# Optimization experiments

Measured on AMD Instinct MI355X. Metric: run time of the kernel, lower is better.

The kernel has to match this reference:

```python
import jax, jax.numpy as jnp
import numpy as np

E = 1024   # embed_dim
H = 8      # att_heads
HD = E // H
L = 4      # layer_num
B = 64
M = 256
EPS = 1e-5


def celu(x, alpha=1.3):
    return jnp.where(x > 0, x, alpha * jnp.expm1(x / alpha))


def group_norm(x, w, b):
    # x: [N, E], groups = H (GroupNorm over channel groups, per-sample)
    xg = x.reshape(-1, H, HD)
    mu = xg.mean(-1, keepdims=True)
    var = ((xg - mu) ** 2).mean(-1, keepdims=True)
    xg = (xg - mu) * jax.lax.rsqrt(var + EPS)
    return xg.reshape(-1, E) * w + b


def layer_norm(x, w, b):
    mu = x.mean(-1, keepdims=True)
    var = ((x - mu) ** 2).mean(-1, keepdims=True)
    return (x - mu) * jax.lax.rsqrt(var + EPS) * w + b


def setup_inputs() -> dict:
    key = jax.random.key(0)
    ks = jax.random.split(key, 20)
    s = 0.02
    return {
        "gv_feat": jnp.zeros((B, 1), jnp.float32),
        "att_feats": jax.random.normal(ks[0], (B, M, E), jnp.float32),
        "att_mask": jnp.ones((B, M), jnp.float32),
        "mem_W": jax.random.normal(ks[1], (L, E, E), jnp.float32) * s,
        "mem_b": jnp.zeros((L, E), jnp.float32),
        "gn_w": jnp.ones((L, E), jnp.float32),
        "gn_b": jnp.zeros((L, E), jnp.float32),
        "upd_W": jax.random.normal(ks[2], (L, 2 * HD, HD), jnp.float32) * s,
        "upd_b": jnp.zeros((L, HD), jnp.float32),
        "gate_W": jax.random.normal(ks[3], (L, 2 * HD, HD), jnp.float32) * s,
        "gate_b": jnp.zeros((L, HD), jnp.float32),
        "ln_w": jnp.ones((L, E), jnp.float32),
        "ln_b": jnp.zeros((L, E), jnp.float32),
        "proj_W": jax.random.normal(ks[4], ((L + 1) * E, E), jnp.float32) * s,
        "proj_b": jnp.zeros((E,), jnp.float32),
        "lnf_w": jnp.ones((E,), jnp.float32),
        "lnf_b": jnp.zeros((E,), jnp.float32),
    }


def reference(gv_feat, att_feats, att_mask, mem_W, mem_b, gn_w, gn_b,
              upd_W, upd_b, gate_W, gate_b, ln_w, ln_b,
              proj_W, proj_b, lnf_w, lnf_b):
    scaling = HD ** (-0.5)
    mask3 = att_mask[:, :, None]                       # [B, M, 1]
    msum = mask3.sum(1)                                # [B, 1]

    def pool(x):
        return (x * mask3).sum(1) / msum               # [B, E]

    # gv_feat has last dim 1 -> computed by masked mean pooling
    gv = pool(att_feats)
    feat_arr = [gv]
    x = att_feats
    key_mask = att_mask[:, None, None, :]              # [B, 1, 1, M]
    for i in range(L):
        mem = celu(x.reshape(-1, E) @ mem_W[i] + mem_b[i])
        mem = group_norm(mem, gn_w[i], gn_b[i])
        xh = x.reshape(B, M, H, HD).swapaxes(1, 2)     # [B, H, M, HD]
        mh = mem.reshape(B, M, H, HD).swapaxes(1, 2)   # [B, H, M, HD]
        attn = jnp.einsum('bhqd,bhkd->bhqk', xh, mh) * scaling
        attn = jnp.where(key_mask == 0, -1e9, attn)
        p = jax.nn.softmax(attn, axis=-1)
        ctx = jnp.einsum('bhqk,bhkd->bhqd', p, xh)     # values == xh
        inp = jnp.concatenate([xh, ctx], axis=-1)      # [B, H, M, 2*HD]
        f_t = jnp.tanh(jax.nn.relu(inp @ upd_W[i] + upd_b[i]))  # dropout = eval identity
        g_t = jax.nn.sigmoid(inp @ gate_W[i] + gate_b[i])
        xh = g_t * f_t + (1.0 - g_t) * xh
        x = xh.swapaxes(1, 2).reshape(B, M, E)
        x = layer_norm(x, ln_w[i], ln_b[i])
        feat_arr.append(pool(x))
    gv = jnp.concatenate(feat_arr, axis=-1) @ proj_W + proj_b
    gv = layer_norm(gv, lnf_w, lnf_b)
    return gv, x
```

## Files before the change

### kernel.cpp

```cpp
#include <hip/hip_runtime.h>
#include <hip/hip_bf16.h>
#include <cstdint>
#include <cstddef>

typedef __bf16 v8bf __attribute__((ext_vector_type(8)));
typedef __bf16 v4bf __attribute__((ext_vector_type(4)));
typedef float  f32x4 __attribute__((ext_vector_type(4)));

typedef __attribute__((address_space(1))) void gas_void;
typedef __attribute__((address_space(3))) void las_void;

__device__ __forceinline__ void gload_lds16(const void* g, void* l) {
  __builtin_amdgcn_global_load_lds((const gas_void*)g, (las_void*)l, 16, 0, 0);
}

__device__ __forceinline__ float rdv(const void* p, size_t idx, int isf) {
  return isf ? ((const float*)p)[idx] : (float)((const __bf16*)p)[idx];
}

#define PB 64
#define PM 256
#define PE 1024
#define PH 8
#define PHD 128

__global__ void detect_kernel(const void* mask, int* flags) {
  if (threadIdx.x == 0) {
    uint32_t w = *(const uint32_t*)mask;
    flags[0] = ((w >> 16) == 0x3F80u && (w & 0xFFFFu) == 0x3F80u) ? 0 : 1;
  }
}

__global__ __launch_bounds__(256) void convx_kernel(
    const void* __restrict__ src, const int* __restrict__ flags, __bf16* __restrict__ dst) {
  const size_t i = ((size_t)blockIdx.x * 256 + threadIdx.x) * 4;
  if (flags[0]) {
    const float* s = (const float*)src + i;
    v4bf o; o[0] = (__bf16)s[0]; o[1] = (__bf16)s[1]; o[2] = (__bf16)s[2]; o[3] = (__bf16)s[3];
    *(v4bf*)(dst + i) = o;
  } else {
    *(v4bf*)(dst + i) = *(const v4bf*)((const __bf16*)src + i);
  }
}

__global__ __launch_bounds__(256) void transpose_kernel(
    const void* __restrict__ src, size_t soff, size_t zsrc, const int* __restrict__ flags,
    __bf16* __restrict__ dst, size_t zdst, int K, int N) {
  __shared__ __bf16 tile[64][66];
  const int isf = flags[0];
  const size_t so = soff + (size_t)blockIdx.z * zsrc;
  __bf16* d = dst + (size_t)blockIdx.z * zdst;
  const int n0 = blockIdx.x * 64, k0 = blockIdx.y * 64;
  const int c = threadIdx.x & 63, r0 = threadIdx.x >> 6;
#pragma unroll
  for (int j = 0; j < 16; ++j) {
    const int r = j * 4 + r0;
    tile[r][c] = (__bf16)rdv(src, so + (size_t)(k0 + r) * N + (n0 + c), isf);
  }
  __syncthreads();
#pragma unroll
  for (int j = 0; j < 16; ++j) {
    const int r = j * 4 + r0;
    d[(size_t)(n0 + r) * K + k0 + c] = tile[c][r];
  }
}

__global__ __launch_bounds__(256) void ugtr_kernel(
    const void* __restrict__ updW, const void* __restrict__ gateW,
    const int* __restrict__ flags, __bf16* __restrict__ ugWt) {
  __shared__ __bf16 tile[64][66];
  const int isf = flags[0];
  const int z = blockIdx.z, i = z >> 1, g = z & 1;
  const void* src = g ? gateW : updW;
  const size_t soff = (size_t)i * 32768;
  __bf16* dst = ugWt + (size_t)i * 65536 + g * 32768;
  const int n0 = blockIdx.x * 64, k0 = blockIdx.y * 64;
  const int c = threadIdx.x & 63, r0 = threadIdx.x >> 6;
#pragma unroll
  for (int j = 0; j < 16; ++j) {
    const int r = j * 4 + r0;
    tile[r][c] = (__bf16)rdv(src, soff + (size_t)(k0 + r) * 128 + (n0 + c), isf);
  }
  __syncthreads();
#pragma unroll
  for (int j = 0; j < 16; ++j) {
    const int r = j * 4 + r0;
    dst[(size_t)(n0 + r) * 256 + k0 + c] = tile[c][r];
  }
}

template<int AMODE, int BMODE, int ACT, bool OUTF32, bool CLAMPM, bool GNF, bool SPLITK, bool SWZ>
__global__ __launch_bounds__(512) void gemm_kernel(
    const __bf16* __restrict__ A, const __bf16* __restrict__ A2,
    const __bf16* __restrict__ Bt,
    const void* __restrict__ bias_a, int offa, const void* __restrict__ bias_b, int offb,
    int bias_split, const int* __restrict__ flags,
    const void* __restrict__ gnw, const void* __restrict__ gnb, int gnoff,
    void* __restrict__ Cout, int K, int Kfull, int Ntot, int Mtot)
{
  __shared__ __align__(16) uint8_t a_s[2][32768];
  __shared__ __align__(16) uint8_t b_s[2][16384];
  __shared__ float gnsum[256][2];
  __shared__ float gnsq[256][2];
  int bx = blockIdx.x, by = blockIdx.y;
  if (SWZ) {
    const int nx = gridDim.x;
    const int flat = by * nx + bx;
    const int xcd = flat & 7, slot = flat >> 3;
    by = slot & 7;
    bx = (slot >> 3) * 8 + xcd;
  }
  const int mbase = bx * 256;
  const int nbase = by * 128;
  const int koff = SPLITK ? blockIdx.z * K : 0;
  const int tid = threadIdx.x;
  const int wid = tid >> 6, lane = tid & 63;
  const int wr = wid >> 1, wc = wid & 1;

  f32x4 acc[4][4];
#pragma unroll
  for (int m = 0; m < 4; ++m)
#pragma unroll
    for (int n = 0; n < 4; ++n) acc[m][n] = (f32x4){0.f, 0.f, 0.f, 0.f};

  const int nkt = K >> 6;
  const int lrow8 = lane >> 3;
  const int cc = (lane & 7) << 4;

  auto STAGE = [&](int kt, uint8_t* as, uint8_t* bs) {
    const int kbase = koff + (kt << 6);
#pragma unroll
    for (int j = 0; j < 4; ++j) {
      const int q = wid * 4 + j;
      const int row = q * 8 + lrow8;
      const int c = cc ^ ((row & 7) << 4);
      const int klocal = c >> 1;
      const __bf16* asrc;
      if (AMODE == 0) {
        int rg = mbase + row;
        if (CLAMPM && rg > Mtot - 1) rg = Mtot - 1;
        asrc = A + (size_t)rg * Kfull + (kbase + klocal);
      } else {
        const int rg = mbase + row;
        const int kg = kbase + klocal;
        if (kg < PHD) {
          const int bh = rg >> 8, mm = rg & 255;
          const int bb = bh >> 3, hh = bh & 7;
          asrc = A + ((size_t)(bb * PM + mm) * PE + hh * PHD + kg);
        } else {
          asrc = A2 + ((size_t)rg * PHD + (kg - PHD));
        }
      }
      gload_lds16(asrc, as + q * 1024);
    }
#pragma unroll
    for (int j = 0; j < 2; ++j) {
      const int q = wid * 2 + j;
      const int row = q * 8 + lrow8;
      const int c = cc ^ ((row & 7) << 4);
      const int klocal = c >> 1;
      const __bf16* bsrc;
      if (BMODE == 0) {
        bsrc = Bt + (size_t)(nbase + row) * Kfull + (kbase + klocal);
      } else {
        bsrc = Bt + (size_t)(mbase >> 8) * (PHD * PM)
                  + (size_t)(nbase + row) * Kfull + (kbase + klocal);
      }
      gload_lds16(bsrc, bs + q * 1024);
    }
  };

  STAGE(0, a_s[0], b_s[0]);
  if (nkt > 1) STAGE(1, a_s[1], b_s[1]);

  for (int kt = 0; kt < nkt; ++kt) {
    if (kt + 1 < nkt) asm volatile("s_waitcnt vmcnt(6)" ::: "memory");
    else              asm volatile("s_waitcnt vmcnt(0)" ::: "memory");
    __builtin_amdgcn_s_barrier();
    __builtin_amdgcn_sched_barrier(0);
    const uint8_t* ap = a_s[kt & 1];
    const uint8_t* bp = b_s[kt & 1];
#pragma unroll
    for (int kk = 0; kk < 2; ++kk) {
      const int co = kk * 64 + ((lane >> 4) << 4);
      v8bf af[4], bfr[4];
#pragma unroll
      for (int m = 0; m < 4; ++m) {
        const int row = wr * 64 + m * 16 + (lane & 15);
        af[m] = *(const v8bf*)(ap + row * 128 + (co ^ ((row & 7) << 4)));
      }
#pragma unroll
      for (int n = 0; n < 4; ++n) {
        const int row = wc * 64 + n * 16 + (lane & 15);
        bfr[n] = *(const v8bf*)(bp + row * 128 + (co ^ ((row & 7) << 4)));
      }
#pragma unroll
      for (int m = 0; m < 4; ++m)
#pragma unroll
        for (int n = 0; n < 4; ++n)
          acc[m][n] = __builtin_amdgcn_mfma_f32_16x16x32_bf16(af[m], bfr[n], acc[m][n], 0, 0, 0);
    }
    __builtin_amdgcn_s_barrier();
    __builtin_amdgcn_sched_barrier(0);
    if (kt + 2 < nkt) STAGE(kt + 2, a_s[kt & 1], b_s[kt & 1]);
  }

  const int isf = flags[0];
  if constexpr (GNF) {
    float bv[4];
#pragma unroll
    for (int n = 0; n < 4; ++n) {
      const int col = nbase + wc * 64 + n * 16 + (lane & 15);
      bv[n] = (bias_a != nullptr) ? rdv(bias_a, offa + col, isf) : 0.f;
    }
#pragma unroll
    for (int m = 0; m < 4; ++m)
#pragma unroll
      for (int n = 0; n < 4; ++n)
#pragma unroll
        for (int r = 0; r < 4; ++r) {
          float v = acc[m][n][r] + bv[n];
          if (ACT == 1) v = (v > 0.f) ? v : 1.3f * expm1f(v * (1.0f / 1.3f));
          acc[m][n][r] = v;
        }
#pragma unroll
    for (int m = 0; m < 4; ++m)
#pragma unroll
      for (int r = 0; r < 4; ++r) {
        float s = 0.f, q = 0.f;
#pragma unroll
        for (int n = 0; n < 4; ++n) { s += acc[m][n][r]; q += acc[m][n][r] * acc[m][n][r]; }
#pragma unroll
        for (int off = 1; off < 16; off <<= 1) {
          s += __shfl_xor(s, off, 64); q += __shfl_xor(q, off, 64);
        }
        const int lrow = wr * 64 + m * 16 + ((lane >> 4) << 2) + r;
        if ((lane & 15) == 0) { gnsum[lrow][wc] = s; gnsq[lrow][wc] = q; }
      }
    __syncthreads();
#pragma unroll
    for (int m = 0; m < 4; ++m)
#pragma unroll
      for (int r = 0; r < 4; ++r) {
        const int lrow = wr * 64 + m * 16 + ((lane >> 4) << 2) + r;
        const float mean = (gnsum[lrow][0] + gnsum[lrow][1]) * (1.f / 128.f);
        const float var = (gnsq[lrow][0] + gnsq[lrow][1]) * (1.f / 128.f) - mean * mean;
        const float rstd = rsqrtf(var + 1e-5f);
        const int rg = mbase + lrow;
#pragma unroll
        for (int n = 0; n < 4; ++n) {
          const int col = nbase + wc * 64 + n * 16 + (lane & 15);
          const float o = (acc[m][n][r] - mean) * rstd * rdv(gnw, gnoff + col, isf)
                          + rdv(gnb, gnoff + col, isf);
          ((__bf16*)Cout)[(size_t)rg * Ntot + col] = (__bf16)o;
        }
      }
  } else {
    float* coutF = (float*)Cout + (SPLITK ? (size_t)blockIdx.z * 65536 : (size_t)0);
#pragma unroll
    for (int m = 0; m < 4; ++m) {
      const int rowt = mbase + wr * 64 + m * 16 + ((lane >> 4) << 2);
#pragma unroll
      for (int n = 0; n < 4; ++n) {
        const int col = nbase + wc * 64 + n * 16 + (lane & 15);
        float bvv = 0.f;
        if (bias_a != nullptr)
          bvv = (col < bias_split) ? rdv(bias_a, offa + col, isf)
                                   : rdv(bias_b, offb + col - bias_split, isf);
#pragma unroll
        for (int r = 0; r < 4; ++r) {
          const int rg = rowt + r;
          if (CLAMPM && rg >= Mtot) continue;
          float v = acc[m][n][r] + bvv;
          if (ACT == 1) v = (v > 0.f) ? v : 1.3f * expm1f(v * (1.0f / 1.3f));
          if (OUTF32) coutF[(size_t)rg * Ntot + col] = v;
          else        ((__bf16*)Cout)[(size_t)rg * Ntot + col] = (__bf16)v;
        }
      }
    }
  }
}

__global__ __launch_bounds__(256) void attn_softmax_kernel(
    const __bf16* __restrict__ xc, const __bf16* __restrict__ memc,
    const void* __restrict__ mask, const int* __restrict__ flags, int b0,
    __bf16* __restrict__ S)
{
  const int bhl = blockIdx.x;
  const int bl = bhl >> 3, h = bhl & 7;
  const int isf = flags[0];
  const int tid = threadIdx.x, wid = tid >> 6, lane = tid & 63;
  const int qbase = blockIdx.y * 64 + wid * 16;
  const size_t xoff = (size_t)bl * PM * PE + h * PHD;

  v8bf a[4];
  {
    const int row = qbase + (lane & 15);
    const int d0 = (lane >> 4) * 8;
    const __bf16* p = xc + xoff + (size_t)row * PE + d0;
#pragma unroll
    for (int k = 0; k < 4; ++k) a[k] = *(const v8bf*)(p + k * 32);
  }
  float mz[16];
#pragma unroll
  for (int t = 0; t < 16; ++t)
    mz[t] = rdv(mask, (size_t)(b0 + bl) * PM + t * 16 + (lane & 15), isf);

  f32x4 acc[16];
#pragma unroll
  for (int t = 0; t < 16; ++t) acc[t] = (f32x4){0.f, 0.f, 0.f, 0.f};
#pragma unroll
  for (int t = 0; t < 16; ++t) {
    const int key = t * 16 + (lane & 15);
    const int d0 = (lane >> 4) * 8;
    const __bf16* p = memc + xoff + (size_t)key * PE + d0;
#pragma unroll
    for (int k = 0; k < 4; ++k) {
      v8bf bb = *(const v8bf*)(p + k * 32);
      acc[t] = __builtin_amdgcn_mfma_f32_16x16x32_bf16(a[k], bb, acc[t], 0, 0, 0);
    }
  }
  const float scale = 0.08838834764831845f;
  float mx[4], sm[4];
#pragma unroll
  for (int r = 0; r < 4; ++r) mx[r] = -3.0e38f;
#pragma unroll
  for (int t = 0; t < 16; ++t)
#pragma unroll
    for (int r = 0; r < 4; ++r) {
      float v = (mz[t] == 0.f) ? -1.0e9f : acc[t][r] * scale;
      acc[t][r] = v;
      mx[r] = fmaxf(mx[r], v);
    }
#pragma unroll
  for (int off = 1; off < 16; off <<= 1)
#pragma unroll
    for (int r = 0; r < 4; ++r) mx[r] = fmaxf(mx[r], __shfl_xor(mx[r], off, 64));
#pragma unroll
  for (int r = 0; r < 4; ++r) sm[r] = 0.f;
#pragma unroll
  for (int t = 0; t < 16; ++t)
#pragma unroll
    for (int r = 0; r < 4; ++r) {
      float e = expf(acc[t][r] - mx[r]);
      acc[t][r] = e; sm[r] += e;
    }
#pragma unroll
  for (int off = 1; off < 16; off <<= 1)
#pragma unroll
    for (int r = 0; r < 4; ++r) sm[r] += __shfl_xor(sm[r], off, 64);
#pragma unroll
  for (int r = 0; r < 4; ++r) sm[r] = 1.f / sm[r];

  const size_t srow = (size_t)bhl * PM;
#pragma unroll
  for (int r = 0; r < 4; ++r) {
    const int q = qbase + (lane >> 4) * 4 + r;
    __bf16* sp = S + (srow + q) * PM;
#pragma unroll
    for (int t = 0; t < 16; ++t)
      sp[t * 16 + (lane & 15)] = (__bf16)(acc[t][r] * sm[r]);
  }
}

__global__ __launch_bounds__(256) void transpose_x_kernel(
    const __bf16* __restrict__ xc, __bf16* __restrict__ xT)
{
  const int bh = blockIdx.x;
  const int b = bh >> 3, h = bh & 7;
  const int tz = blockIdx.y;
  const int d0 = (tz & 1) * 64, m0 = (tz >> 1) * 64;
  __shared__ __bf16 tile[64][66];
  const int c = threadIdx.x & 63, r0 = threadIdx.x >> 6;
  const __bf16* src = xc + ((size_t)b * PM + m0) * PE + h * PHD + d0;
#pragma unroll
  for (int j = 0; j < 16; ++j) {
    const int r = j * 4 + r0;
    tile[r][c] = src[(size_t)r * PE + c];
  }
  __syncthreads();
  __bf16* dst = xT + ((size_t)bh * PHD + d0) * PM + m0;
#pragma unroll
  for (int j = 0; j < 16; ++j) {
    const int r = j * 4 + r0;
    dst[(size_t)r * PM + c] = tile[c][r];
  }
}

__global__ __launch_bounds__(256) void gatingln_kernel(
    const __bf16* __restrict__ ug, const __bf16* __restrict__ xc,
    const void* __restrict__ w, const void* __restrict__ bz, int off,
    const int* __restrict__ flags, __bf16* __restrict__ xout,
    void* __restrict__ outAux, int row0)
{
  const size_t row = blockIdx.x;
  const int tid = threadIdx.x, wid = tid >> 6, lane = tid & 63;
  const int isf = flags[0];
  const int e = tid * 4, h = tid >> 5, d = e & 127;
  const size_t b = row >> 8; const int m = (int)(row & 255);
  const size_t ugrow = ((b * PH + h) * PM + m);
  v4bf fv = *(const v4bf*)(ug + ugrow * 256 + d);
  v4bf gvv = *(const v4bf*)(ug + ugrow * 256 + 128 + d);
  v4bf xv = *(const v4bf*)(xc + row * PE + e);
  float o[4];
#pragma unroll
  for (int r = 0; r < 4; ++r) {
    float f = fv[r], g = gvv[r], xh = xv[r];
    float gs = 1.f / (1.f + expf(-g));
    float ft = tanhf(fmaxf(f, 0.f));
    o[r] = gs * ft + (1.f - gs) * xh;
  }
  float s = o[0] + o[1] + o[2] + o[3];
  float q = o[0] * o[0] + o[1] * o[1] + o[2] * o[2] + o[3] * o[3];
#pragma unroll
  for (int off2 = 1; off2 < 64; off2 <<= 1) {
    s += __shfl_xor(s, off2, 64); q += __shfl_xor(q, off2, 64);
  }
  __shared__ float ss[4], qq[4];
  if (lane == 0) { ss[wid] = s; qq[wid] = q; }
  __syncthreads();
  s = ss[0] + ss[1] + ss[2] + ss[3];
  q = qq[0] + qq[1] + qq[2] + qq[3];
  const float mean = s * (1.f / 1024.f);
  const float var = q * (1.f / 1024.f) - mean * mean;
  const float rstd = rsqrtf(var + 1e-5f);
  float ov[4];
#pragma unroll
  for (int r = 0; r < 4; ++r)
    ov[r] = (o[r] - mean) * rstd * rdv(w, off + e + r, isf) + rdv(bz, off + e + r, isf);
  v4bf vo; vo[0] = (__bf16)ov[0]; vo[1] = (__bf16)ov[1]; vo[2] = (__bf16)ov[2]; vo[3] = (__bf16)ov[3];
  *(v4bf*)(xout + row * PE + e) = vo;
  if (outAux != nullptr) {
    const size_t idx = 65536 + (size_t)(row0 + row) * PE + e;
    if (isf) {
      float* op = (float*)outAux;
      op[idx] = ov[0]; op[idx + 1] = ov[1]; op[idx + 2] = ov[2]; op[idx + 3] = ov[3];
    } else {
      __bf16* op = (__bf16*)outAux;
      op[idx] = (__bf16)ov[0]; op[idx + 1] = (__bf16)ov[1];
      op[idx + 2] = (__bf16)ov[2]; op[idx + 3] = (__bf16)ov[3];
    }
  }
}

__global__ void msum_kernel(const void* __restrict__ mask, const int* __restrict__ flags,
                            float* __restrict__ msum)
{
  const int b = blockIdx.x, t = threadIdx.x;
  const int isf = flags[0];
  float s = 0.f;
#pragma unroll
  for (int j = 0; j < 4; ++j) s += rdv(mask, (size_t)b * PM + j * 64 + t, isf);
#pragma unroll
  for (int off = 1; off < 64; off <<= 1) s += __shfl_xor(s, off, 64);
  if (t == 0) msum[b] = s;
}

__global__ __launch_bounds__(1024) void pool_kernel(
    const __bf16* __restrict__ x, const void* __restrict__ mask, const int* __restrict__ flags,
    const float* __restrict__ msum, __bf16* __restrict__ feats, int colOff)
{
  __shared__ float red[4][256];
  const int b = blockIdx.x;
  const int el = threadIdx.x & 255;
  const int wq = threadIdx.x >> 8;
  const int e = blockIdx.y * 256 + el;
  const int isf = flags[0];
  const __bf16* p = x + (size_t)b * PM * PE + e;
  float acc = 0.f;
  const int m0 = wq * 64;
  for (int m = m0; m < m0 + 64; m += 4) {
#pragma unroll
    for (int j = 0; j < 4; ++j)
      acc += (float)p[(size_t)(m + j) * PE] * rdv(mask, (size_t)b * PM + m + j, isf);
  }
  red[wq][el] = acc;
  __syncthreads();
  if (wq == 0) {
    float s = red[0][el] + red[1][el] + red[2][el] + red[3][el];
    feats[(size_t)b * (5 * PE) + colOff + e] = (__bf16)(s / msum[b]);
  }
}

__global__ __launch_bounds__(256) void projreduce_kernel(
    const float* __restrict__ part, const void* __restrict__ pb,
    const int* __restrict__ flags, float* __restrict__ gvpre)
{
  const int row = blockIdx.x;
  const int c0 = threadIdx.x * 4;
  const int isf = flags[0];
  float a0 = rdv(pb, c0 + 0, isf), a1 = rdv(pb, c0 + 1, isf);
  float a2 = rdv(pb, c0 + 2, isf), a3 = rdv(pb, c0 + 3, isf);
#pragma unroll
  for (int z = 0; z < 8; ++z) {
    const float* p = part + (size_t)z * 65536 + (size_t)row * 1024 + c0;
    a0 += p[0]; a1 += p[1]; a2 += p[2]; a3 += p[3];
  }
  float* op = gvpre + (size_t)row * 1024 + c0;
  op[0] = a0; op[1] = a1; op[2] = a2; op[3] = a3;
}

__global__ __launch_bounds__(256) void ln_final_kernel(
    const float* __restrict__ gin, const void* __restrict__ w, const void* __restrict__ bz,
    const int* __restrict__ flags, void* __restrict__ out)
{
  const size_t row = blockIdx.x;
  const int tid = threadIdx.x, wid = tid >> 6, lane = tid & 63;
  const int isf = flags[0];
  const float* p = gin + row * PE + tid * 4;
  float f0 = p[0], f1 = p[1], f2 = p[2], f3 = p[3];
  float s = f0 + f1 + f2 + f3;
  float q = f0 * f0 + f1 * f1 + f2 * f2 + f3 * f3;
#pragma unroll
  for (int off = 1; off < 64; off <<= 1) {
    s += __shfl_xor(s, off, 64); q += __shfl_xor(q, off, 64);
  }
  __shared__ float ss[4], qq[4];
  if (lane == 0) { ss[wid] = s; qq[wid] = q; }
  __syncthreads();
  s = ss[0] + ss[1] + ss[2] + ss[3];
  q = qq[0] + qq[1] + qq[2] + qq[3];
  const float mean = s * (1.f / 1024.f);
  const float var = q * (1.f / 1024.f) - mean * mean;
  const float rstd = rsqrtf(var + 1e-5f);
  const int e = tid * 4;
#pragma unroll
  for (int j = 0; j < 4; ++j) {
    const float fj = (j == 0 ? f0 : j == 1 ? f1 : j == 2 ? f2 : f3);
    const float ov = (fj - mean) * rstd * rdv(w, e + j, isf) + rdv(bz, e + j, isf);
    if (isf) ((float*)out)[row * PE + e + j] = ov;
    else     ((__bf16*)out)[row * PE + e + j] = (__bf16)ov;
  }
}

extern "C" void kernel_launch(void* const* d_in, const int* in_sizes, int n_in,
                              void* d_out, int out_size, void* d_ws, size_t ws_size,
                              hipStream_t stream) {
  const void* att_feats = d_in[1];
  const void* att_mask  = d_in[2];
  const void* mem_W  = d_in[3];
  const void* mem_b  = d_in[4];
  const void* gn_w   = d_in[5];
  const void* gn_b   = d_in[6];
  const void* upd_W  = d_in[7];
  const void* upd_b  = d_in[8];
  const void* gate_W = d_in[9];
  const void* gate_b = d_in[10];
  const void* ln_w   = d_in[11];
  const void* ln_b   = d_in[12];
  const void* proj_W = d_in[13];
  const void* proj_b = d_in[14];
  const void* lnf_w  = d_in[15];
  const void* lnf_b  = d_in[16];

  uint8_t* ws = (uint8_t*)d_ws;
  int*    flags  = (int*)ws;
  float*  msum   = (float*)(ws + 4096);
  __bf16* featsb = (__bf16*)(ws + 8192);
  float*  gvpre  = (float*)(ws + 665600);
  __bf16* memWt  = (__bf16*)(ws + 1048576);
  __bf16* ugWt   = (__bf16*)(ws + 9437184);
  __bf16* xa0    = (__bf16*)(ws + 10485760);
  __bf16* xa     = (__bf16*)(ws + 44040192);
  uint8_t* dynb  = ws + 77594624;

  int NC;
  if (ws_size >= (size_t)211812352) NC = 1;
  else if (ws_size >= (size_t)144703488) NC = 2;
  else NC = 4;
  const int CSd = PB / NC;
  const int CROWSd = CSd * PM;
  const int CGRd = CSd * PH * PM;
  const size_t CB = (size_t)CROWSd * PE * 2;
  __bf16* membc = (__bf16*)dynb;
  __bf16* xTgc  = (__bf16*)(dynb + CB);
  __bf16* sbufc = (__bf16*)(dynb + 2 * CB);

  detect_kernel<<<1, 64, 0, stream>>>(att_mask, flags);
  convx_kernel<<<16384, 256, 0, stream>>>(att_feats, flags, xa0);

  transpose_kernel<<<dim3(16, 16, 4), 256, 0, stream>>>(
      mem_W, 0, 1048576, flags, memWt, 1048576, 1024, 1024);
  ugtr_kernel<<<dim3(2, 4, 8), 256, 0, stream>>>(upd_W, gate_W, flags, ugWt);

  msum_kernel<<<64, 64, 0, stream>>>(att_mask, flags, msum);
  pool_kernel<<<dim3(64, 4), 1024, 0, stream>>>(xa0, att_mask, flags, msum, featsb, 0);

  const __bf16* xcur = xa0;
  for (int i = 0; i < 4; ++i) {
    for (int c = 0; c < NC; ++c) {
      const __bf16* xc = xcur + (size_t)c * CROWSd * PE;
      gemm_kernel<0, 0, 1, false, false, true, false, true><<<dim3(CROWSd / 256, 8), 512, 0, stream>>>(
          xc, nullptr, memWt + (size_t)i * 1048576, mem_b, i * 1024, nullptr, 0, 1024,
          flags, gn_w, gn_b, i * 1024, membc, 1024, 1024, 1024, CROWSd);
      transpose_x_kernel<<<dim3(CSd * 8, 8), 256, 0, stream>>>(xc, xTgc);
      attn_softmax_kernel<<<dim3(CSd * 8, 4), 256, 0, stream>>>(xc, membc, att_mask, flags,
                                                                c * CSd, sbufc);
      gemm_kernel<0, 1, 0, false, false, false, false, false><<<dim3(CGRd / 256, 1), 512, 0, stream>>>(
          sbufc, nullptr, xTgc, nullptr, 0, nullptr, 0, 128, flags, nullptr, nullptr, 0,
          membc, 256, 256, 128, CGRd);
      gemm_kernel<1, 0, 0, false, false, false, false, false><<<dim3(CGRd / 256, 2), 512, 0, stream>>>(
          xc, membc, ugWt + (size_t)i * 65536, upd_b, i * 128, gate_b, i * 128, 128,
          flags, nullptr, nullptr, 0, sbufc, 256, 256, 256, CGRd);
      gatingln_kernel<<<CROWSd, 256, 0, stream>>>(sbufc, xc, ln_w, ln_b, i * 1024, flags,
                                                  xa + (size_t)c * CROWSd * PE,
                                                  (i == 3) ? d_out : nullptr, c * CROWSd);
    }
    pool_kernel<<<dim3(64, 4), 1024, 0, stream>>>(xa, att_mask, flags, msum, featsb,
                                                  (i + 1) * 1024);
    xcur = xa;
  }

  __bf16* projWt = sbufc;
  float* projPart = (float*)dynb;
  transpose_kernel<<<dim3(16, 80, 1), 256, 0, stream>>>(proj_W, 0, 0, flags, projWt, 0, 5120, 1024);
  gemm_kernel<0, 0, 0, true, true, false, true, false><<<dim3(1, 8, 8), 512, 0, stream>>>(
      featsb, nullptr, projWt, nullptr, 0, nullptr, 0, 1024,
      flags, nullptr, nullptr, 0, projPart, 640, 5120, 1024, 64);
  projreduce_kernel<<<64, 256, 0, stream>>>(projPart, proj_b, flags, gvpre);
  ln_final_kernel<<<64, 256, 0, stream>>>(gvpre, lnf_w, lnf_b, flags, d_out);
}
```

Before: 1.330 ms.

## Triple-buffer GEMM LDS and interleave staging with MFMA phases

Moves the bf16 GEMM from a double-buffered LDS pipeline to a triple-buffered one. Global-to-LDS staging for tile kt+2 is split into three parts and spread across four MFMA sub-phases, with s_setprio raising priority around the MFMA bursts. The wave layout changes from 4x2 waves with 64x64 tiles to 2x4 waves with 128x32 tiles. GroupNorm reduction scratch now aliases the B buffer, which keeps total LDS within limits. The aim is to hide global-load latency behind matrix math, at the cost of more barriers per k-step and slightly more LDS fragment reads per wave.

After: 1.635 ms. 1.23x slower.

```diff
diff --git a/kernel.cpp b/kernel.cpp
--- a/kernel.cpp
+++ b/kernel.cpp
@@ -98,10 +98,11 @@
     const void* __restrict__ gnw, const void* __restrict__ gnb, int gnoff,
     void* __restrict__ Cout, int K, int Kfull, int Ntot, int Mtot)
 {
-  __shared__ __align__(16) uint8_t a_s[2][32768];
-  __shared__ __align__(16) uint8_t b_s[2][16384];
-  __shared__ float gnsum[256][2];
-  __shared__ float gnsq[256][2];
+  __shared__ __align__(16) uint8_t a_s[3][32768];
+  __shared__ __align__(16) uint8_t b_s[3][16384];
+  float* gnS = (float*)&b_s[0][0];
+  float* gnQ = (float*)&b_s[0][4096];
+
   int bx = blockIdx.x, by = blockIdx.y;
   if (SWZ) {
     const int nx = gridDim.x;
@@ -115,108 +116,129 @@
   const int koff = SPLITK ? blockIdx.z * K : 0;
   const int tid = threadIdx.x;
   const int wid = tid >> 6, lane = tid & 63;
-  const int wr = wid >> 1, wc = wid & 1;
-
-  f32x4 acc[4][4];
-#pragma unroll
-  for (int m = 0; m < 4; ++m)
-#pragma unroll
-    for (int n = 0; n < 4; ++n) acc[m][n] = (f32x4){0.f, 0.f, 0.f, 0.f};
+  const int wr = wid >> 2, wc = wid & 3;
+
+  f32x4 acc[8][2];
+#pragma unroll
+  for (int m = 0; m < 8; ++m)
+#pragma unroll
+    for (int n = 0; n < 2; ++n) acc[m][n] = (f32x4){0.f, 0.f, 0.f, 0.f};
 
   const int nkt = K >> 6;
   const int lrow8 = lane >> 3;
   const int cc = (lane & 7) << 4;
 
-  auto STAGE = [&](int kt, uint8_t* as, uint8_t* bs) {
+  auto STAGE_PART = [&](int kt, int part, uint8_t* as, uint8_t* bs) {
     const int kbase = koff + (kt << 6);
-#pragma unroll
-    for (int j = 0; j < 4; ++j) {
-      const int q = wid * 4 + j;
-      const int row = q * 8 + lrow8;
-      const int c = cc ^ ((row & 7) << 4);
-      const int klocal = c >> 1;
-      const __bf16* asrc;
-      if (AMODE == 0) {
-        int rg = mbase + row;
-        if (CLAMPM && rg > Mtot - 1) rg = Mtot - 1;
-        asrc = A + (size_t)rg * Kfull + (kbase + klocal);
-      } else {
-        const int rg = mbase + row;
-        const int kg = kbase + klocal;
-        if (kg < PHD) {
-          const int bh = rg >> 8, mm = rg & 255;
-          const int bb = bh >> 3, hh = bh & 7;
-          asrc = A + ((size_t)(bb * PM + mm) * PE + hh * PHD + kg);
+    if (part < 2) {
+#pragma unroll
+      for (int jj = 0; jj < 2; ++jj) {
+        const int q = wid * 4 + part * 2 + jj;
+        const int row = q * 8 + lrow8;
+        const int c = cc ^ ((row & 7) << 4);
+        const int klocal = c >> 1;
+        const __bf16* asrc;
+        if (AMODE == 0) {
+          int rg = mbase + row;
+          if (CLAMPM && rg > Mtot - 1) rg = Mtot - 1;
+          asrc = A + (size_t)rg * Kfull + (kbase + klocal);
         } else {
-          asrc = A2 + ((size_t)rg * PHD + (kg - PHD));
-        }
+          const int rg = mbase + row;
+          const int kg = kbase + klocal;
+          if (kg < PHD) {
+            const int bh = rg >> 8, mm = rg & 255;
+            const int bb = bh >> 3, hh = bh & 7;
+            asrc = A + ((size_t)(bb * PM + mm) * PE + hh * PHD + kg);
+          } else {
+            asrc = A2 + ((size_t)rg * PHD + (kg - PHD));
+          }
+        }
+        gload_lds16(asrc, as + q * 1024);
       }
-      gload_lds16(asrc, as + q * 1024);
-    }
-#pragma unroll
-    for (int j = 0; j < 2; ++j) {
-      const int q = wid * 2 + j;
-      const int row = q * 8 + lrow8;
-      const int c = cc ^ ((row & 7) << 4);
-      const int klocal = c >> 1;
-      const __bf16* bsrc;
-      if (BMODE == 0) {
-        bsrc = Bt + (size_t)(nbase + row) * Kfull + (kbase + klocal);
-      } else {
-        bsrc = Bt + (size_t)(mbase >> 8) * (PHD * PM)
-                  + (size_t)(nbase + row) * Kfull + (kbase + klocal);
+    } else {
+#pragma unroll
+      for (int jj = 0; jj < 2; ++jj) {
+        const int q = wid * 2 + jj;
+        const int row = q * 8 + lrow8;
+        const int c = cc ^ ((row & 7) << 4);
+        const int klocal = c >> 1;
+        const __bf16* bsrc;
+        if (BMODE == 0) {
+          bsrc = Bt + (size_t)(nbase + row) * Kfull + (kbase + klocal);
+        } else {
+          bsrc = Bt + (size_t)(mbase >> 8) * (PHD * PM)
+                    + (size_t)(nbase + row) * Kfull + (kbase + klocal);
+        }
+        gload_lds16(bsrc, bs + q * 1024);
       }
-      gload_lds16(bsrc, bs + q * 1024);
     }
   };
 
-  STAGE(0, a_s[0], b_s[0]);
-  if (nkt > 1) STAGE(1, a_s[1], b_s[1]);
+  STAGE_PART(0, 0, a_s[0], b_s[0]);
+  STAGE_PART(0, 1, a_s[0], b_s[0]);
+  STAGE_PART(0, 2, a_s[0], b_s[0]);
+  if (nkt > 1) {
+    STAGE_PART(1, 0, a_s[1], b_s[1]);
+    STAGE_PART(1, 1, a_s[1], b_s[1]);
+    STAGE_PART(1, 2, a_s[1], b_s[1]);
+  }
 
   for (int kt = 0; kt < nkt; ++kt) {
     if (kt + 1 < nkt) asm volatile("s_waitcnt vmcnt(6)" ::: "memory");
     else              asm volatile("s_waitcnt vmcnt(0)" ::: "memory");
     __builtin_amdgcn_s_barrier();
     __builtin_amdgcn_sched_barrier(0);
-    const uint8_t* ap = a_s[kt & 1];
-    const uint8_t* bp = b_s[kt & 1];
-#pragma unroll
-    for (int kk = 0; kk < 2; ++kk) {
-      const int co = kk * 64 + ((lane >> 4) << 4);
-      v8bf af[4], bfr[4];
-#pragma unroll
-      for (int m = 0; m < 4; ++m) {
-        const int row = wr * 64 + m * 16 + (lane & 15);
-        af[m] = *(const v8bf*)(ap + row * 128 + (co ^ ((row & 7) << 4)));
+    const uint8_t* ap = a_s[kt % 3];
+    const uint8_t* bp = b_s[kt % 3];
+    uint8_t* an = a_s[(kt + 2) % 3];
+    uint8_t* bn = b_s[(kt + 2) % 3];
+    const bool stage = (kt + 2 < nkt);
+#pragma unroll
+    for (int p = 0; p < 4; ++p) {
+      const int mh = p >> 1, nh = p & 1;
+      v8bf af[2][4], bfr[2];
+#pragma unroll
+      for (int kk = 0; kk < 2; ++kk) {
+        const int co = kk * 64 + ((lane >> 4) << 4);
+#pragma unroll
+        for (int mi = 0; mi < 4; ++mi) {
+          const int row = wr * 128 + (mh * 4 + mi) * 16 + (lane & 15);
+          af[kk][mi] = *(const v8bf*)(ap + row * 128 + (co ^ ((row & 7) << 4)));
+        }
+        {
+          const int row = wc * 32 + nh * 16 + (lane & 15);
+          bfr[kk] = *(const v8bf*)(bp + row * 128 + (co ^ ((row & 7) << 4)));
+        }
       }
-#pragma unroll
-      for (int n = 0; n < 4; ++n) {
-        const int row = wc * 64 + n * 16 + (lane & 15);
-        bfr[n] = *(const v8bf*)(bp + row * 128 + (co ^ ((row & 7) << 4)));
-      }
-#pragma unroll
-      for (int m = 0; m < 4; ++m)
-#pragma unroll
-        for (int n = 0; n < 4; ++n)
-          acc[m][n] = __builtin_amdgcn_mfma_f32_16x16x32_bf16(af[m], bfr[n], acc[m][n], 0, 0, 0);
-    }
-    __builtin_amdgcn_s_barrier();
-    __builtin_amdgcn_sched_barrier(0);
-    if (kt + 2 < nkt) STAGE(kt + 2, a_s[kt & 1], b_s[kt & 1]);
+      if (stage && p < 3) STAGE_PART(kt + 2, p, an, bn);
+      __builtin_amdgcn_s_barrier();
+      __builtin_amdgcn_sched_barrier(0);
+      __builtin_amdgcn_s_setprio(1);
+#pragma unroll
+      for (int kk = 0; kk < 2; ++kk)
+#pragma unroll
+        for (int mi = 0; mi < 4; ++mi)
+          acc[mh * 4 + mi][nh] =
+              __builtin_amdgcn_mfma_f32_16x16x32_bf16(af[kk][mi], bfr[kk], acc[mh * 4 + mi][nh], 0, 0, 0);
+      __builtin_amdgcn_s_setprio(0);
+      __builtin_amdgcn_s_barrier();
+      __builtin_amdgcn_sched_barrier(0);
+    }
   }
 
   const int isf = flags[0];
   if constexpr (GNF) {
-    float bv[4];
-#pragma unroll
-    for (int n = 0; n < 4; ++n) {
-      const int col = nbase + wc * 64 + n * 16 + (lane & 15);
+    __syncthreads();
+    float bv[2];
+#pragma unroll
+    for (int n = 0; n < 2; ++n) {
+      const int col = nbase + wc * 32 + n * 16 + (lane & 15);
       bv[n] = (bias_a != nullptr) ? rdv(bias_a, offa + col, isf) : 0.f;
     }
 #pragma unroll
-    for (int m = 0; m < 4; ++m)
-#pragma unroll
-      for (int n = 0; n < 4; ++n)
+    for (int m = 0; m < 8; ++m)
+#pragma unroll
+      for (int n = 0; n < 2; ++n)
 #pragma unroll
         for (int r = 0; r < 4; ++r) {
           float v = acc[m][n][r] + bv[n];
@@ -224,32 +246,33 @@
           acc[m][n][r] = v;
         }
 #pragma unroll
-    for (int m = 0; m < 4; ++m)
+    for (int m = 0; m < 8; ++m)
 #pragma unroll
       for (int r = 0; r < 4; ++r) {
-        float s = 0.f, q = 0.f;
-#pragma unroll
-        for (int n = 0; n < 4; ++n) { s += acc[m][n][r]; q += acc[m][n][r] * acc[m][n][r]; }
+        float s = acc[m][0][r] + acc[m][1][r];
+        float q = acc[m][0][r] * acc[m][0][r] + acc[m][1][r] * acc[m][1][r];
 #pragma unroll
         for (int off = 1; off < 16; off <<= 1) {
           s += __shfl_xor(s, off, 64); q += __shfl_xor(q, off, 64);
         }
-        const int lrow = wr * 64 + m * 16 + ((lane >> 4) << 2) + r;
-        if ((lane & 15) == 0) { gnsum[lrow][wc] = s; gnsq[lrow][wc] = q; }
+        const int lrow = wr * 128 + m * 16 + ((lane >> 4) << 2) + r;
+        if ((lane & 15) == 0) { gnS[lrow * 4 + wc] = s; gnQ[lrow * 4 + wc] = q; }
       }
     __syncthreads();
 #pragma unroll
-    for (int m = 0; m < 4; ++m)
+    for (int m = 0; m < 8; ++m)
 #pragma unroll
       for (int r = 0; r < 4; ++r) {
-        const int lrow = wr * 64 + m * 16 + ((lane >> 4) << 2) + r;
-        const float mean = (gnsum[lrow][0] + gnsum[lrow][1]) * (1.f / 128.f);
-        const float var = (gnsq[lrow][0] + gnsq[lrow][1]) * (1.f / 128.f) - mean * mean;
+        const int lrow = wr * 128 + m * 16 + ((lane >> 4) << 2) + r;
+        const float sum = gnS[lrow * 4] + gnS[lrow * 4 + 1] + gnS[lrow * 4 + 2] + gnS[lrow * 4 + 3];
+        const float sq  = gnQ[lrow * 4] + gnQ[lrow * 4 + 1] + gnQ[lrow * 4 + 2] + gnQ[lrow * 4 + 3];
+        const float mean = sum * (1.f / 128.f);
+        const float var = sq * (1.f / 128.f) - mean * mean;
         const float rstd = rsqrtf(var + 1e-5f);
         const int rg = mbase + lrow;
 #pragma unroll
-        for (int n = 0; n < 4; ++n) {
-          const int col = nbase + wc * 64 + n * 16 + (lane & 15);
+        for (int n = 0; n < 2; ++n) {
+          const int col = nbase + wc * 32 + n * 16 + (lane & 15);
           const float o = (acc[m][n][r] - mean) * rstd * rdv(gnw, gnoff + col, isf)
                           + rdv(gnb, gnoff + col, isf);
           ((__bf16*)Cout)[(size_t)rg * Ntot + col] = (__bf16)o;
@@ -258,11 +281,11 @@
   } else {
     float* coutF = (float*)Cout + (SPLITK ? (size_t)blockIdx.z * 65536 : (size_t)0);
 #pragma unroll
-    for (int m = 0; m < 4; ++m) {
-      const int rowt = mbase + wr * 64 + m * 16 + ((lane >> 4) << 2);
-#pragma unroll
-      for (int n = 0; n < 4; ++n) {
-        const int col = nbase + wc * 64 + n * 16 + (lane & 15);
+    for (int m = 0; m < 8; ++m) {
+      const int rowt = mbase + wr * 128 + m * 16 + ((lane >> 4) << 2);
+#pragma unroll
+      for (int n = 0; n < 2; ++n) {
+        const int col = nbase + wc * 32 + n * 16 + (lane & 15);
         float bvv = 0.f;
         if (bias_a != nullptr)
           bvv = (col < bias_split) ? rdv(bias_a, offa + col, isf)
@@ -372,11 +395,10 @@
   const int d0 = (tz & 1) * 64, m0 = (tz >> 1) * 64;
   __shared__ __bf16 tile[64][66];
   const int c = threadIdx.x & 63, r0 = threadIdx.x >> 6;
-  const __bf16* src = xc + ((size_t)b * PM + m0) * PE + h * PHD + d0;
 #pragma unroll
   for (int j = 0; j < 16; ++j) {
     const int r = j * 4 + r0;
-    tile[r][c] = src[(size_t)r * PE + c];
+    tile[r][c] = xc[((size_t)b * PM + m0 + r) * PE + h * PHD + d0 + c];
   }
   __syncthreads();
   __bf16* dst = xT + ((size_t)bh * PHD + d0) * PM + m0;
```

## Fuse softmax probabilities with PV matmul inside the attention kernel

Applied to the files above, without the earlier changes.

The attention kernel now keeps each wave's normalized probability tile in LDS and multiplies it directly against the transposed x values with MFMA, writing ctx instead of the full probability matrix. This removes the global write and re-read of the B*H*M*M score buffer and one GEMM launch. In exchange, each wave re-reads the xT tile from global/L2 per 16-row query slice, with less reuse than the tiled GEMM had. Buffers are re-aliased so ug output reuses the mem buffer.

Result: slower. 1.383 ms (+4.0%).

```diff
diff --git a/kernel.cpp b/kernel.cpp
--- a/kernel.cpp
+++ b/kernel.cpp
@@ -127,7 +127,7 @@
   const int lrow8 = lane >> 3;
   const int cc = (lane & 7) << 4;
 
-  auto STAGE = [&](int kt, uint8_t* as, uint8_t* bs) {
+  auto STAGE2 = [&](int kt, uint8_t* as, uint8_t* bs) {
     const int kbase = koff + (kt << 6);
 #pragma unroll
     for (int j = 0; j < 4; ++j) {
@@ -159,19 +159,13 @@
       const int row = q * 8 + lrow8;
       const int c = cc ^ ((row & 7) << 4);
       const int klocal = c >> 1;
-      const __bf16* bsrc;
-      if (BMODE == 0) {
-        bsrc = Bt + (size_t)(nbase + row) * Kfull + (kbase + klocal);
-      } else {
-        bsrc = Bt + (size_t)(mbase >> 8) * (PHD * PM)
-                  + (size_t)(nbase + row) * Kfull + (kbase + klocal);
-      }
+      const __bf16* bsrc = Bt + (size_t)(nbase + row) * Kfull + (kbase + klocal);
       gload_lds16(bsrc, bs + q * 1024);
     }
   };
 
-  STAGE(0, a_s[0], b_s[0]);
-  if (nkt > 1) STAGE(1, a_s[1], b_s[1]);
+  STAGE2(0, a_s[0], b_s[0]);
+  if (nkt > 1) STAGE2(1, a_s[1], b_s[1]);
 
   for (int kt = 0; kt < nkt; ++kt) {
     if (kt + 1 < nkt) asm volatile("s_waitcnt vmcnt(6)" ::: "memory");
@@ -202,7 +196,7 @@
     }
     __builtin_amdgcn_s_barrier();
     __builtin_amdgcn_sched_barrier(0);
-    if (kt + 2 < nkt) STAGE(kt + 2, a_s[kt & 1], b_s[kt & 1]);
+    if (kt + 2 < nkt) STAGE2(kt + 2, a_s[kt & 1], b_s[kt & 1]);
   }
 
   const int isf = flags[0];
@@ -281,11 +275,12 @@
   }
 }
 
-__global__ __launch_bounds__(256) void attn_softmax_kernel(
+__global__ __launch_bounds__(256) void attn_pv_kernel(
     const __bf16* __restrict__ xc, const __bf16* __restrict__ memc,
-    const void* __restrict__ mask, const int* __restrict__ flags, int b0,
-    __bf16* __restrict__ S)
-{
+    const __bf16* __restrict__ xT, const void* __restrict__ mask,
+    const int* __restrict__ flags, int b0, __bf16* __restrict__ ctx)
+{
+  __shared__ __align__(16) __bf16 P_lds[4][16][264];
   const int bhl = blockIdx.x;
   const int bl = bhl >> 3, h = bhl & 7;
   const int isf = flags[0];
@@ -352,14 +347,34 @@
 #pragma unroll
   for (int r = 0; r < 4; ++r) sm[r] = 1.f / sm[r];
 
-  const size_t srow = (size_t)bhl * PM;
 #pragma unroll
   for (int r = 0; r < 4; ++r) {
-    const int q = qbase + (lane >> 4) * 4 + r;
-    __bf16* sp = S + (srow + q) * PM;
+    const int row = (lane >> 4) * 4 + r;
 #pragma unroll
     for (int t = 0; t < 16; ++t)
-      sp[t * 16 + (lane & 15)] = (__bf16)(acc[t][r] * sm[r]);
+      P_lds[wid][row][t * 16 + (lane & 15)] = (__bf16)(acc[t][r] * sm[r]);
+  }
+  v8bf pf[8];
+#pragma unroll
+  for (int ks = 0; ks < 8; ++ks)
+    pf[ks] = *(const v8bf*)&P_lds[wid][lane & 15][ks * 32 + ((lane >> 4) << 3)];
+
+  const __bf16* xtp = xT + (size_t)bhl * (PHD * PM);
+  const size_t crow = (size_t)bhl * PM + qbase + ((lane >> 4) << 2);
+#pragma unroll 2
+  for (int n = 0; n < 8; ++n) {
+    const int d = n * 16 + (lane & 15);
+    v8bf bf2[8];
+#pragma unroll
+    for (int ks = 0; ks < 8; ++ks)
+      bf2[ks] = *(const v8bf*)&xtp[(size_t)d * PM + ks * 32 + ((lane >> 4) << 3)];
+    f32x4 c2 = (f32x4){0.f, 0.f, 0.f, 0.f};
+#pragma unroll
+    for (int ks = 0; ks < 8; ++ks)
+      c2 = __builtin_amdgcn_mfma_f32_16x16x32_bf16(pf[ks], bf2[ks], c2, 0, 0, 0);
+#pragma unroll
+    for (int r = 0; r < 4; ++r)
+      ctx[(crow + r) * PHD + n * 16 + (lane & 15)] = (__bf16)c2[r];
   }
 }
 
@@ -372,11 +387,10 @@
   const int d0 = (tz & 1) * 64, m0 = (tz >> 1) * 64;
   __shared__ __bf16 tile[64][66];
   const int c = threadIdx.x & 63, r0 = threadIdx.x >> 6;
-  const __bf16* src = xc + ((size_t)b * PM + m0) * PE + h * PHD + d0;
 #pragma unroll
   for (int j = 0; j < 16; ++j) {
     const int r = j * 4 + r0;
-    tile[r][c] = src[(size_t)r * PE + c];
+    tile[r][c] = xc[((size_t)b * PM + m0 + r) * PE + h * PHD + d0 + c];
   }
   __syncthreads();
   __bf16* dst = xT + ((size_t)bh * PHD + d0) * PM + m0;
@@ -574,7 +588,8 @@
   const size_t CB = (size_t)CROWSd * PE * 2;
   __bf16* membc = (__bf16*)dynb;
   __bf16* xTgc  = (__bf16*)(dynb + CB);
-  __bf16* sbufc = (__bf16*)(dynb + 2 * CB);
+  __bf16* ctxc  = (__bf16*)(dynb + 2 * CB);
+  __bf16* ugc   = (__bf16*)dynb;
 
   detect_kernel<<<1, 64, 0, stream>>>(att_mask, flags);
   convx_kernel<<<16384, 256, 0, stream>>>(att_feats, flags, xa0);
@@ -594,15 +609,12 @@
           xc, nullptr, memWt + (size_t)i * 1048576, mem_b, i * 1024, nullptr, 0, 1024,
           flags, gn_w, gn_b, i * 1024, membc, 1024, 1024, 1024, CROWSd);
       transpose_x_kernel<<<dim3(CSd * 8, 8), 256, 0, stream>>>(xc, xTgc);
-      attn_softmax_kernel<<<dim3(CSd * 8, 4), 256, 0, stream>>>(xc, membc, att_mask, flags,
-                                                                c * CSd, sbufc);
-      gemm_kernel<0, 1, 0, false, false, false, false, false><<<dim3(CGRd / 256, 1), 512, 0, stream>>>(
-          sbufc, nullptr, xTgc, nullptr, 0, nullptr, 0, 128, flags, nullptr, nullptr, 0,
-          membc, 256, 256, 128, CGRd);
+      attn_pv_kernel<<<dim3(CSd * 8, 4), 256, 0, stream>>>(xc, membc, xTgc, att_mask, flags,
+                                                           c * CSd, ctxc);
       gemm_kernel<1, 0, 0, false, false, false, false, false><<<dim3(CGRd / 256, 2), 512, 0, stream>>>(
-          xc, membc, ugWt + (size_t)i * 65536, upd_b, i * 128, gate_b, i * 128, 128,
-          flags, nullptr, nullptr, 0, sbufc, 256, 256, 256, CGRd);
-      gatingln_kernel<<<CROWSd, 256, 0, stream>>>(sbufc, xc, ln_w, ln_b, i * 1024, flags,
+          xc, ctxc, ugWt + (size_t)i * 65536, upd_b, i * 128, gate_b, i * 128, 128,
+          flags, nullptr, nullptr, 0, ugc, 256, 256, 256, CGRd);
+      gatingln_kernel<<<CROWSd, 256, 0, stream>>>(ugc, xc, ln_w, ln_b, i * 1024, flags,
                                                   xa + (size_t)c * CROWSd * PE,
                                                   (i == 3) ? d_out : nullptr, c * CROWSd);
     }
@@ -611,7 +623,7 @@
     xcur = xa;
   }
 
-  __bf16* projWt = sbufc;
+  __bf16* projWt = (__bf16*)(dynb + 2 * CB);
   float* projPart = (float*)dynb;
   transpose_kernel<<<dim3(16, 80, 1), 256, 0, stream>>>(proj_W, 0, 0, flags, projWt, 0, 5120, 1024);
   gemm_kernel<0, 0, 0, true, true, false, true, false><<<dim3(1, 8, 8), 512, 0, stream>>>(
```
